# Performance work log

Measured on AMD Instinct MI355X. Metric: run time of the kernel, lower is better.

The kernel has to match this reference:

```python
import jax, jax.numpy as jnp
import numpy as np

B, H, S, D = 4, 16, 2048, 64


def setup_inputs() -> dict:
    key = jax.random.key(0)
    kq, kk, kv = jax.random.split(key, 3)
    q = jax.random.normal(kq, (B, H, S, D), dtype=jnp.float32)
    k = jax.random.normal(kk, (B, H, S, D), dtype=jnp.float32)
    v = jax.random.normal(kv, (B, H, S, D), dtype=jnp.float32)
    mask = jnp.tril(jnp.ones((S, S), dtype=jnp.bool_))  # causal: True = attend
    return {"q": q, "k": k, "v": v, "mask": mask}


def reference(q, k, v, mask):
    d_k = q.shape[-1]
    scale = 1.0 / jnp.sqrt(jnp.asarray(d_k, q.dtype))
    # scores: [B, H, S_q, S_k] -- full O(N^2) matrix, faithful to original
    score = jnp.einsum('bhqd,bhkd->bhqk', q, k) * scale
    score = jnp.where(mask, score, jnp.asarray(-jnp.inf, score.dtype))
    attn = jax.nn.softmax(score, axis=-1)
    return jnp.einsum('bhqk,bhkd->bhqd', attn, v)
```

## Files before the change

kernel.cpp:

```cpp
#include <hip/hip_runtime.h>
#include <hip/hip_bf16.h>

typedef __attribute__((ext_vector_type(8))) short short8_t;
typedef __attribute__((ext_vector_type(16))) float f32x16;
typedef __attribute__((ext_vector_type(4))) unsigned uint4_t;

constexpr int S  = 2048;
constexpr int D  = 64;
constexpr int BQ = 128;
constexpr int KV = 64;
constexpr int NQ = S / BQ;
constexpr int NT = S / KV;
constexpr float THR = 8.f;

static __device__ __forceinline__ unsigned packbf(float lo, float hi) {
  __hip_bfloat162 p = __float22bfloat162_rn(float2{lo, hi});
  return (unsigned)__bfloat16_as_ushort(p.x) | ((unsigned)__bfloat16_as_ushort(p.y) << 16);
}
static __device__ __forceinline__ short8_t pack8(float4 a, float4 b) {
  uint4_t u = { packbf(a.x, a.y), packbf(a.z, a.w), packbf(b.x, b.y), packbf(b.z, b.w) };
  return __builtin_bit_cast(short8_t, u);
}
static __device__ __forceinline__ float vmax16(const f32x16& a) {
  float x0 = fmaxf(a[0], a[1]),   x1 = fmaxf(a[2], a[3]);
  float x2 = fmaxf(a[4], a[5]),   x3 = fmaxf(a[6], a[7]);
  float x4 = fmaxf(a[8], a[9]),   x5 = fmaxf(a[10], a[11]);
  float x6 = fmaxf(a[12], a[13]), x7 = fmaxf(a[14], a[15]);
  x0 = fmaxf(x0, x1); x2 = fmaxf(x2, x3); x4 = fmaxf(x4, x5); x6 = fmaxf(x6, x7);
  return fmaxf(fmaxf(x0, x2), fmaxf(x4, x6));
}

static __device__ __forceinline__ void build_pfrags(const f32x16& p, int h,
                                                    short8_t& f0, short8_t& f1) {
  unsigned W0 = packbf(p[0],  p[1]),  W1 = packbf(p[2],  p[3]);
  unsigned W2 = packbf(p[4],  p[5]),  W3 = packbf(p[6],  p[7]);
  unsigned W4 = packbf(p[8],  p[9]),  W5 = packbf(p[10], p[11]);
  unsigned W6 = packbf(p[12], p[13]), W7 = packbf(p[14], p[15]);
  unsigned e0 = __shfl_xor(W0, 32), e1 = __shfl_xor(W1, 32);
  unsigned e2 = __shfl_xor(W2, 32), e3 = __shfl_xor(W3, 32);
  unsigned e4 = __shfl_xor(W4, 32), e5 = __shfl_xor(W5, 32);
  unsigned e6 = __shfl_xor(W6, 32), e7 = __shfl_xor(W7, 32);
  uint4_t u0, u1;
  if (h) { u0 = uint4_t{e2, e3, W2, W3}; u1 = uint4_t{e6, e7, W6, W7}; }
  else   { u0 = uint4_t{W0, W1, e0, e1}; u1 = uint4_t{W4, W5, e4, e5}; }
  f0 = __builtin_bit_cast(short8_t, u0);
  f1 = __builtin_bit_cast(short8_t, u1);
}

__global__ __launch_bounds__(256)
void prep_kernel(const float* __restrict__ k, const float* __restrict__ v,
                 short* __restrict__ kb, short* __restrict__ vtb)
{
  const int tile = (int)blockIdx.x;
  const int bh   = (int)blockIdx.y;
  const int tid  = (int)threadIdx.x;
  const int kv0  = tile * KV;
  const int srow = tid >> 2, sch = tid & 3;

  __shared__ float vt[KV][D + 4];

  {
    const float* kp = k + ((size_t)bh * S + kv0 + srow) * D + sch * 16;
    float4 a0 = *(const float4*)(kp);     float4 a1 = *(const float4*)(kp + 4);
    float4 a2 = *(const float4*)(kp + 8); float4 a3 = *(const float4*)(kp + 12);
    short* kd = kb + ((size_t)bh * S + kv0 + srow) * D;
    *(short8_t*)&kd[((2 * sch)     ^ (srow & 7)) * 8] = pack8(a0, a1);
    *(short8_t*)&kd[((2 * sch + 1) ^ (srow & 7)) * 8] = pack8(a2, a3);

    const float* vp = v + ((size_t)bh * S + kv0 + srow) * D + sch * 16;
    float4 b0 = *(const float4*)(vp);     float4 b1 = *(const float4*)(vp + 4);
    float4 b2 = *(const float4*)(vp + 8); float4 b3 = *(const float4*)(vp + 12);
    *(float4*)&vt[srow][sch * 16 + 0]  = b0;
    *(float4*)&vt[srow][sch * 16 + 4]  = b1;
    *(float4*)&vt[srow][sch * 16 + 8]  = b2;
    *(float4*)&vt[srow][sch * 16 + 12] = b3;
  }
  __syncthreads();
  {
    const int d = tid >> 2, q4 = tid & 3;
    float f[16];
    #pragma unroll
    for (int jj = 0; jj < 16; ++jj) f[jj] = vt[16 * q4 + jj][d];
    float4 c0 = make_float4(f[0],  f[1],  f[2],  f[3]);
    float4 c1 = make_float4(f[4],  f[5],  f[6],  f[7]);
    float4 c2 = make_float4(f[8],  f[9],  f[10], f[11]);
    float4 c3 = make_float4(f[12], f[13], f[14], f[15]);
    short* vd = vtb + (size_t)bh * S * D + (size_t)tile * KV * D + d * 64;
    *(short8_t*)&vd[((2 * q4)     ^ (d & 7)) * 8] = pack8(c0, c1);
    *(short8_t*)&vd[((2 * q4 + 1) ^ (d & 7)) * 8] = pack8(c2, c3);
  }
}

__global__ __launch_bounds__(256, 2)
void fattn4_kernel(const float* __restrict__ q, const short* __restrict__ kb,
                   const short* __restrict__ vtb, float* __restrict__ out)
{
  const int pair = (int)blockIdx.x;
  const int bh   = (int)blockIdx.y;
  const int tid  = (int)threadIdx.x;
  const int wave = tid >> 6;
  const int lane = tid & 63;
  const int h    = lane >> 5;
  const int ln   = lane & 31;

  __shared__ short bufK[2][KV * D];
  __shared__ short bufV[2][KV * D];

  const int nt0 = 2 * (pair + 1);
  const int ntt = nt0 + 2 * (NQ - pair);
  const short* kbase = kb  + (size_t)bh * S * D;
  const short* vbase = vtb + (size_t)bh * S * D;

  short8_t rk0, rk1, rv0, rv1;
  auto issue = [&](int t) {
    const short* gk = kbase + (size_t)t * (KV * D) + tid * 16;
    rk0 = *(const short8_t*)gk; rk1 = *(const short8_t*)(gk + 8);
    const short* gv = vbase + (size_t)t * (KV * D) + tid * 16;
    rv0 = *(const short8_t*)gv; rv1 = *(const short8_t*)(gv + 8);
  };
  issue(0);
  int cur = 0, j = 0;

  const float qscale = 0.125f * 1.4426950408889634f;

  #pragma unroll 1
  for (int seg = 0; seg < 2; ++seg) {
    const int qblk = seg ? (NQ - 1 - pair) : pair;
    const int qb = qblk * BQ;
    const int qw = qb + wave * 32;
    const int qi = qw + ln;
    const int qmax_w = qw + 31;
    const int ntseg = 2 * (qblk + 1);

    short8_t aq[4];
    {
      const float* qp = q + ((size_t)bh * S + qi) * D + 8 * h;
      #pragma unroll
      for (int ks = 0; ks < 4; ++ks) {
        float4 lo = *(const float4*)(qp + 16 * ks);
        float4 hi = *(const float4*)(qp + 16 * ks + 4);
        lo.x *= qscale; lo.y *= qscale; lo.z *= qscale; lo.w *= qscale;
        hi.x *= qscale; hi.y *= qscale; hi.z *= qscale; hi.w *= qscale;
        aq[ks] = pack8(lo, hi);
      }
    }

    f32x16 o0, o1;
    #pragma unroll
    for (int r = 0; r < 16; ++r) { o0[r] = 0.f; o1[r] = 0.f; }
    float m = -INFINITY, lsum = 0.f;

    #pragma unroll 1
    for (int i = 0; i < ntseg; ++i) {
      {
        short* dK = &bufK[cur][tid * 16];
        *(short8_t*)dK = rk0; *(short8_t*)(dK + 8) = rk1;
        short* dV = &bufV[cur][tid * 16];
        *(short8_t*)dV = rv0; *(short8_t*)(dV + 8) = rv1;
      }
      ++j;
      if (j < ntt) issue(j < nt0 ? j : j - nt0);
      __syncthreads();

      const int kv0 = i * KV;
      if (kv0 <= qmax_w) {
        const bool hi_live = (kv0 + 32 <= qmax_w);
        const short* Kc = bufK[cur];
        const short* Vc = bufV[cur];

        f32x16 st0, st1;
        #pragma unroll
        for (int r = 0; r < 16; ++r) { st0[r] = 0.f; st1[r] = 0.f; }
        #pragma unroll
        for (int ks = 0; ks < 4; ++ks) {
          short8_t kf0 = *(const short8_t*)&Kc[ln * D + (((2 * ks + h) ^ (ln & 7)) * 8)];
          st0 = __builtin_amdgcn_mfma_f32_32x32x16_bf16(kf0, aq[ks], st0, 0, 0, 0);
        }
        if (hi_live) {
          #pragma unroll
          for (int ks = 0; ks < 4; ++ks) {
            short8_t kf1 = *(const short8_t*)&Kc[(32 + ln) * D + (((2 * ks + h) ^ (ln & 7)) * 8)];
            st1 = __builtin_amdgcn_mfma_f32_32x32x16_bf16(kf1, aq[ks], st1, 0, 0, 0);
          }
        }

        if (kv0 + KV - 1 > qw) {
          #pragma unroll
          for (int r = 0; r < 16; ++r) {
            const int kvr = kv0 + (r & 3) + 8 * (r >> 2) + 4 * h;
            st0[r] = (kvr > qi) ? -INFINITY : st0[r];
            if (hi_live) st1[r] = (kvr + 32 > qi) ? -INFINITY : st1[r];
          }
        }

        float tm = hi_live ? fmaxf(vmax16(st0), vmax16(st1)) : vmax16(st0);
        tm = fmaxf(tm, __shfl_xor(tm, 32));
        if (!__all(tm <= m + THR)) {
          const float mn = fmaxf(m, tm);
          const float al = exp2f(m - mn);
          m = mn;
          lsum *= al;
          #pragma unroll
          for (int r = 0; r < 16; ++r) { o0[r] *= al; o1[r] *= al; }
        }
        float ssum = 0.f;
        #pragma unroll
        for (int r = 0; r < 16; ++r) { st0[r] = exp2f(st0[r] - m); ssum += st0[r]; }
        if (hi_live) {
          #pragma unroll
          for (int r = 0; r < 16; ++r) { st1[r] = exp2f(st1[r] - m); ssum += st1[r]; }
        }
        ssum += __shfl_xor(ssum, 32);
        lsum += ssum;

        short8_t p00, p01, p10, p11;
        build_pfrags(st0, h, p00, p01);
        if (hi_live) build_pfrags(st1, h, p10, p11);
        #pragma unroll
        for (int dt = 0; dt < 2; ++dt) {
          const int dr = 32 * dt + ln;
          f32x16 &o = dt ? o1 : o0;
          short8_t vf00 = *(const short8_t*)&Vc[dr * 64 + (((0 + h) ^ (dr & 7)) * 8)];
          short8_t vf01 = *(const short8_t*)&Vc[dr * 64 + (((2 + h) ^ (dr & 7)) * 8)];
          o = __builtin_amdgcn_mfma_f32_32x32x16_bf16(vf00, p00, o, 0, 0, 0);
          o = __builtin_amdgcn_mfma_f32_32x32x16_bf16(vf01, p01, o, 0, 0, 0);
          if (hi_live) {
            short8_t vf10 = *(const short8_t*)&Vc[dr * 64 + (((4 + h) ^ (dr & 7)) * 8)];
            short8_t vf11 = *(const short8_t*)&Vc[dr * 64 + (((6 + h) ^ (dr & 7)) * 8)];
            o = __builtin_amdgcn_mfma_f32_32x32x16_bf16(vf10, p10, o, 0, 0, 0);
            o = __builtin_amdgcn_mfma_f32_32x32x16_bf16(vf11, p11, o, 0, 0, 0);
          }
        }
      }
      cur ^= 1;
    }

    const float inv = 1.f / fmaxf(lsum, 1e-37f);
    float* op = out + ((size_t)bh * S + qi) * D;
    #pragma unroll
    for (int r = 0; r < 16; ++r) {
      const int dr = (r & 3) + 8 * (r >> 2) + 4 * h;
      op[dr]      = o0[r] * inv;
      op[32 + dr] = o1[r] * inv;
    }
  }
}

__global__ __launch_bounds__(256, 2)
void fattn3_kernel(const float* __restrict__ q, const float* __restrict__ k,
                   const float* __restrict__ v, float* __restrict__ out)
{
  const int pair = (int)blockIdx.x;
  const int bh   = (int)blockIdx.y;
  const int tid  = (int)threadIdx.x;
  const int wave = tid >> 6;
  const int lane = tid & 63;
  const int h    = lane >> 5;
  const int ln   = lane & 31;

  __shared__ short smem[BQ * D];
  short* Ks = smem;
  short* Vs = smem + KV * D;

  const float qscale = 0.125f * 1.4426950408889634f;
  const int srow = tid >> 2;
  const int sch  = tid & 3;

  #pragma unroll 1
  for (int seg = 0; seg < 2; ++seg) {
    const int qblk = seg ? (NQ - 1 - pair) : pair;
    const int qb = qblk * BQ;
    const int qw = qb + wave * 32;
    const int qi = qw + ln;
    const int qmax_w = qw + 31;
    const int kv_end = qb + BQ;

    __syncthreads();
    {
      const int r  = tid >> 1;
      const int h2 = tid & 1;
      const float* qp = q + ((size_t)bh * S + qb + r) * D + h2 * 32;
      #pragma unroll
      for (int jq = 0; jq < 4; ++jq) {
        float4 a = *(const float4*)(qp + jq * 8);
        float4 b = *(const float4*)(qp + jq * 8 + 4);
        a.x *= qscale; a.y *= qscale; a.z *= qscale; a.w *= qscale;
        b.x *= qscale; b.y *= qscale; b.z *= qscale; b.w *= qscale;
        *(short8_t*)&smem[r * D + (((4 * h2 + jq) ^ (r & 7)) * 8)] = pack8(a, b);
      }
    }
    __syncthreads();

    short8_t aq[4];
    {
      const int R = wave * 32 + ln;
      #pragma unroll
      for (int ks = 0; ks < 4; ++ks)
        aq[ks] = *(const short8_t*)&smem[R * D + (((2 * ks + h) ^ (R & 7)) * 8)];
    }
    __syncthreads();

    f32x16 o0, o1;
    #pragma unroll
    for (int r = 0; r < 16; ++r) { o0[r] = 0.f; o1[r] = 0.f; }
    float m = -INFINITY, lsum = 0.f;

    for (int kv0 = 0; kv0 < kv_end; kv0 += KV) {
      const float* kp = k + ((size_t)bh * S + kv0 + srow) * D + sch * 16;
      const float* vp = v + ((size_t)bh * S + kv0 + srow) * D + sch * 16;
      float4 k0 = *(const float4*)(kp);     float4 k1 = *(const float4*)(kp + 4);
      float4 k2 = *(const float4*)(kp + 8); float4 k3 = *(const float4*)(kp + 12);
      float4 v0 = *(const float4*)(vp);     float4 v1 = *(const float4*)(vp + 4);
      float4 v2 = *(const float4*)(vp + 8); float4 v3 = *(const float4*)(vp + 12);

      __syncthreads();
      *(short8_t*)&Ks[srow * D + (((2 * sch)     ^ (srow & 7)) * 8)] = pack8(k0, k1);
      *(short8_t*)&Ks[srow * D + (((2 * sch + 1) ^ (srow & 7)) * 8)] = pack8(k2, k3);
      {
        float vf[16] = { v0.x,v0.y,v0.z,v0.w, v1.x,v1.y,v1.z,v1.w,
                         v2.x,v2.y,v2.z,v2.w, v3.x,v3.y,v3.z,v3.w };
        #pragma unroll
        for (int jv = 0; jv < 16; jv += 2) {
          const unsigned pw = packbf(vf[jv], vf[jv + 1]);
          const int d0 = 16 * sch + jv, d1 = d0 + 1;
          Vs[d0 * 64 + (((srow >> 3) ^ (d0 & 7)) * 8) + (srow & 7)] = (short)(pw & 0xffffu);
          Vs[d1 * 64 + (((srow >> 3) ^ (d1 & 7)) * 8) + (srow & 7)] = (short)(pw >> 16);
        }
      }
      __syncthreads();

      if (kv0 <= qmax_w) {
        const bool hi_live = (kv0 + 32 <= qmax_w);
        f32x16 st0, st1;
        #pragma unroll
        for (int r = 0; r < 16; ++r) { st0[r] = 0.f; st1[r] = 0.f; }
        #pragma unroll
        for (int ks = 0; ks < 4; ++ks) {
          short8_t kf0 = *(const short8_t*)&Ks[ln * D + (((2 * ks + h) ^ (ln & 7)) * 8)];
          st0 = __builtin_amdgcn_mfma_f32_32x32x16_bf16(kf0, aq[ks], st0, 0, 0, 0);
        }
        if (hi_live) {
          #pragma unroll
          for (int ks = 0; ks < 4; ++ks) {
            short8_t kf1 = *(const short8_t*)&Ks[(32 + ln) * D + (((2 * ks + h) ^ (ln & 7)) * 8)];
            st1 = __builtin_amdgcn_mfma_f32_32x32x16_bf16(kf1, aq[ks], st1, 0, 0, 0);
          }
        }
        if (kv0 + KV - 1 > qw) {
          #pragma unroll
          for (int r = 0; r < 16; ++r) {
            const int kvr = kv0 + (r & 3) + 8 * (r >> 2) + 4 * h;
            st0[r] = (kvr > qi) ? -INFINITY : st0[r];
            if (hi_live) st1[r] = (kvr + 32 > qi) ? -INFINITY : st1[r];
          }
        }
        float tm = hi_live ? fmaxf(vmax16(st0), vmax16(st1)) : vmax16(st0);
        tm = fmaxf(tm, __shfl_xor(tm, 32));
        if (!__all(tm <= m + THR)) {
          const float mn = fmaxf(m, tm);
          const float al = exp2f(m - mn);
          m = mn;
          lsum *= al;
          #pragma unroll
          for (int r = 0; r < 16; ++r) { o0[r] *= al; o1[r] *= al; }
        }
        float ssum = 0.f;
        #pragma unroll
        for (int r = 0; r < 16; ++r) { st0[r] = exp2f(st0[r] - m); ssum += st0[r]; }
        if (hi_live) {
          #pragma unroll
          for (int r = 0; r < 16; ++r) { st1[r] = exp2f(st1[r] - m); ssum += st1[r]; }
        }
        ssum += __shfl_xor(ssum, 32);
        lsum += ssum;

        short8_t p00, p01, p10, p11;
        build_pfrags(st0, h, p00, p01);
        if (hi_live) build_pfrags(st1, h, p10, p11);
        #pragma unroll
        for (int dt = 0; dt < 2; ++dt) {
          const int dr = 32 * dt + ln;
          f32x16 &o = dt ? o1 : o0;
          short8_t vf00 = *(const short8_t*)&Vs[dr * 64 + (((0 + h) ^ (dr & 7)) * 8)];
          short8_t vf01 = *(const short8_t*)&Vs[dr * 64 + (((2 + h) ^ (dr & 7)) * 8)];
          o = __builtin_amdgcn_mfma_f32_32x32x16_bf16(vf00, p00, o, 0, 0, 0);
          o = __builtin_amdgcn_mfma_f32_32x32x16_bf16(vf01, p01, o, 0, 0, 0);
          if (hi_live) {
            short8_t vf10 = *(const short8_t*)&Vs[dr * 64 + (((4 + h) ^ (dr & 7)) * 8)];
            short8_t vf11 = *(const short8_t*)&Vs[dr * 64 + (((6 + h) ^ (dr & 7)) * 8)];
            o = __builtin_amdgcn_mfma_f32_32x32x16_bf16(vf10, p10, o, 0, 0, 0);
            o = __builtin_amdgcn_mfma_f32_32x32x16_bf16(vf11, p11, o, 0, 0, 0);
          }
        }
      }
    }

    const float inv = 1.f / fmaxf(lsum, 1e-37f);
    float* op = out + ((size_t)bh * S + qi) * D;
    #pragma unroll
    for (int r = 0; r < 16; ++r) {
      const int dr = (r & 3) + 8 * (r >> 2) + 4 * h;
      op[dr]      = o0[r] * inv;
      op[32 + dr] = o1[r] * inv;
    }
  }
}

extern "C" void kernel_launch(void* const* d_in, const int* in_sizes, int n_in,
                              void* d_out, int out_size, void* d_ws, size_t ws_size,
                              hipStream_t stream) {
  const float* q = (const float*)d_in[0];
  const float* k = (const float*)d_in[1];
  const float* v = (const float*)d_in[2];
  float* out = (float*)d_out;
  const int BH = in_sizes[0] / (S * D);
  const size_t need = (size_t)BH * S * D * 2  * 2 ;
  if (ws_size >= need) {
    short* kbw  = (short*)d_ws;
    short* vtbw = kbw + (size_t)BH * S * D;
    prep_kernel<<<dim3(NT, BH), 256, 0, stream>>>(k, v, kbw, vtbw);
    fattn4_kernel<<<dim3(NQ / 2, BH), 256, 0, stream>>>(q, kbw, vtbw, out);
  } else {
    fattn3_kernel<<<dim3(NQ / 2, BH), 256, 0, stream>>>(q, k, v, out);
  }
}
```

Baseline: 103.4 us.

## Double query rows per wave to reuse K/V tiles across two Q subtiles

The main attention kernel now assigns 64 query rows per wave (two 32-row subtiles A and B), so each query block grows to 256 rows. Each K fragment loaded from LDS and each V fragment is reused for two MFMA chains, which halves shared-memory reads per FLOP and halves the number of times K/V tiles are streamed per head. The causal mask is simplified to a diagonal-tile check. In exchange it doubles accumulator registers (risking occupancy or spills under the 2-block launch bound), halves the grid to 4 blocks per head (256 blocks total), and makes causal load balancing coarser.

```diff
diff --git a/kernel.cpp b/kernel.cpp
--- a/kernel.cpp
+++ b/kernel.cpp
@@ -7,11 +7,13 @@
 
 constexpr int S  = 2048;
 constexpr int D  = 64;
-constexpr int BQ = 128;
 constexpr int KV = 64;
-constexpr int NQ = S / BQ;
 constexpr int NT = S / KV;
+constexpr int BH_C = 64;
 constexpr float THR = 8.f;
+
+constexpr int BQ7 = 256;
+constexpr int NQ7 = S / BQ7;
 
 static __device__ __forceinline__ unsigned packbf(float lo, float hi) {
   __hip_bfloat162 p = __float22bfloat162_rn(float2{lo, hi});
@@ -47,6 +49,30 @@
   f1 = __builtin_bit_cast(short8_t, u1);
 }
 
+static __device__ __forceinline__ void online_sm(f32x16& st0, f32x16& st1, bool hi,
+                                                 float& m, float& lsum,
+                                                 f32x16& o0, f32x16& o1) {
+  float tm = hi ? fmaxf(vmax16(st0), vmax16(st1)) : vmax16(st0);
+  tm = fmaxf(tm, __shfl_xor(tm, 32));
+  if (!__all(tm <= m + THR)) {
+    const float mn = fmaxf(m, tm);
+    const float al = exp2f(m - mn);
+    m = mn;
+    lsum *= al;
+    #pragma unroll
+    for (int r = 0; r < 16; ++r) { o0[r] *= al; o1[r] *= al; }
+  }
+  float ssum = 0.f;
+  #pragma unroll
+  for (int r = 0; r < 16; ++r) { st0[r] = exp2f(st0[r] - m); ssum += st0[r]; }
+  if (hi) {
+    #pragma unroll
+    for (int r = 0; r < 16; ++r) { st1[r] = exp2f(st1[r] - m); ssum += st1[r]; }
+  }
+  ssum += __shfl_xor(ssum, 32);
+  lsum += ssum;
+}
+
 __global__ __launch_bounds__(256)
 void prep_kernel(const float* __restrict__ k, const float* __restrict__ v,
                  short* __restrict__ kb, short* __restrict__ vtb)
@@ -92,7 +118,7 @@
 }
 
 __global__ __launch_bounds__(256, 2)
-void fattn4_kernel(const float* __restrict__ q, const short* __restrict__ kb,
+void fattn7_kernel(const float* __restrict__ q, const short* __restrict__ kb,
                    const short* __restrict__ vtb, float* __restrict__ out)
 {
   const int pair = (int)blockIdx.x;
@@ -106,8 +132,8 @@
   __shared__ short bufK[2][KV * D];
   __shared__ short bufV[2][KV * D];
 
-  const int nt0 = 2 * (pair + 1);
-  const int ntt = nt0 + 2 * (NQ - pair);
+  const int nt0 = 4 * (pair + 1);
+  const int ntt = nt0 + 4 * (8 - pair);
   const short* kbase = kb  + (size_t)bh * S * D;
   const short* vbase = vtb + (size_t)bh * S * D;
 
@@ -125,30 +151,40 @@
 
   #pragma unroll 1
   for (int seg = 0; seg < 2; ++seg) {
-    const int qblk = seg ? (NQ - 1 - pair) : pair;
-    const int qb = qblk * BQ;
-    const int qw = qb + wave * 32;
-    const int qi = qw + ln;
-    const int qmax_w = qw + 31;
-    const int ntseg = 2 * (qblk + 1);
-
-    short8_t aq[4];
+    const int qblk = seg ? (7 - pair) : pair;
+    const int qb = qblk * BQ7;
+    const int qw = qb + wave * 64;
+    const int qA = qw + ln;
+    const int qB = qw + 32 + ln;
+    const int ntseg = 4 * (qblk + 1);
+    const int nlive = (qw >> 6) + 1;
+
+    short8_t aqA[4], aqB[4];
     {
-      const float* qp = q + ((size_t)bh * S + qi) * D + 8 * h;
+      const float* qpA = q + ((size_t)bh * S + qA) * D + 8 * h;
+      const float* qpB = q + ((size_t)bh * S + qB) * D + 8 * h;
       #pragma unroll
       for (int ks = 0; ks < 4; ++ks) {
-        float4 lo = *(const float4*)(qp + 16 * ks);
-        float4 hi = *(const float4*)(qp + 16 * ks + 4);
+        float4 lo = *(const float4*)(qpA + 16 * ks);
+        float4 hi = *(const float4*)(qpA + 16 * ks + 4);
         lo.x *= qscale; lo.y *= qscale; lo.z *= qscale; lo.w *= qscale;
         hi.x *= qscale; hi.y *= qscale; hi.z *= qscale; hi.w *= qscale;
-        aq[ks] = pack8(lo, hi);
-      }
-    }
-
-    f32x16 o0, o1;
-    #pragma unroll
-    for (int r = 0; r < 16; ++r) { o0[r] = 0.f; o1[r] = 0.f; }
-    float m = -INFINITY, lsum = 0.f;
+        aqA[ks] = pack8(lo, hi);
+      }
+      #pragma unroll
+      for (int ks = 0; ks < 4; ++ks) {
+        float4 lo = *(const float4*)(qpB + 16 * ks);
+        float4 hi = *(const float4*)(qpB + 16 * ks + 4);
+        lo.x *= qscale; lo.y *= qscale; lo.z *= qscale; lo.w *= qscale;
+        hi.x *= qscale; hi.y *= qscale; hi.z *= qscale; hi.w *= qscale;
+        aqB[ks] = pack8(lo, hi);
+      }
+    }
+
+    f32x16 oA0, oA1, oB0, oB1;
+    #pragma unroll
+    for (int r = 0; r < 16; ++r) { oA0[r] = 0.f; oA1[r] = 0.f; oB0[r] = 0.f; oB1[r] = 0.f; }
+    float mA = -INFINITY, lA = 0.f, mB = -INFINITY, lB = 0.f;
 
     #pragma unroll 1
     for (int i = 0; i < ntseg; ++i) {
@@ -162,86 +198,108 @@
       if (j < ntt) issue(j < nt0 ? j : j - nt0);
       __syncthreads();
 
-      const int kv0 = i * KV;
-      if (kv0 <= qmax_w) {
-        const bool hi_live = (kv0 + 32 <= qmax_w);
+      if (i < nlive) {
+        const bool diag = (i == nlive - 1);
         const short* Kc = bufK[cur];
         const short* Vc = bufV[cur];
 
-        f32x16 st0, st1;
-        #pragma unroll
-        for (int r = 0; r < 16; ++r) { st0[r] = 0.f; st1[r] = 0.f; }
-        #pragma unroll
-        for (int ks = 0; ks < 4; ++ks) {
-          short8_t kf0 = *(const short8_t*)&Kc[ln * D + (((2 * ks + h) ^ (ln & 7)) * 8)];
-          st0 = __builtin_amdgcn_mfma_f32_32x32x16_bf16(kf0, aq[ks], st0, 0, 0, 0);
-        }
-        if (hi_live) {
-          #pragma unroll
-          for (int ks = 0; ks < 4; ++ks) {
-            short8_t kf1 = *(const short8_t*)&Kc[(32 + ln) * D + (((2 * ks + h) ^ (ln & 7)) * 8)];
-            st1 = __builtin_amdgcn_mfma_f32_32x32x16_bf16(kf1, aq[ks], st1, 0, 0, 0);
-          }
-        }
-
-        if (kv0 + KV - 1 > qw) {
-          #pragma unroll
-          for (int r = 0; r < 16; ++r) {
-            const int kvr = kv0 + (r & 3) + 8 * (r >> 2) + 4 * h;
-            st0[r] = (kvr > qi) ? -INFINITY : st0[r];
-            if (hi_live) st1[r] = (kvr + 32 > qi) ? -INFINITY : st1[r];
-          }
-        }
-
-        float tm = hi_live ? fmaxf(vmax16(st0), vmax16(st1)) : vmax16(st0);
-        tm = fmaxf(tm, __shfl_xor(tm, 32));
-        if (!__all(tm <= m + THR)) {
-          const float mn = fmaxf(m, tm);
-          const float al = exp2f(m - mn);
-          m = mn;
-          lsum *= al;
-          #pragma unroll
-          for (int r = 0; r < 16; ++r) { o0[r] *= al; o1[r] *= al; }
-        }
-        float ssum = 0.f;
-        #pragma unroll
-        for (int r = 0; r < 16; ++r) { st0[r] = exp2f(st0[r] - m); ssum += st0[r]; }
-        if (hi_live) {
-          #pragma unroll
-          for (int r = 0; r < 16; ++r) { st1[r] = exp2f(st1[r] - m); ssum += st1[r]; }
-        }
-        ssum += __shfl_xor(ssum, 32);
-        lsum += ssum;
-
-        short8_t p00, p01, p10, p11;
-        build_pfrags(st0, h, p00, p01);
-        if (hi_live) build_pfrags(st1, h, p10, p11);
+        short8_t kf0[4], kf1[4];
+        #pragma unroll
+        for (int ks = 0; ks < 4; ++ks)
+          kf0[ks] = *(const short8_t*)&Kc[ln * D + (((2 * ks + h) ^ (ln & 7)) * 8)];
+        #pragma unroll
+        for (int ks = 0; ks < 4; ++ks)
+          kf1[ks] = *(const short8_t*)&Kc[(32 + ln) * D + (((2 * ks + h) ^ (ln & 7)) * 8)];
+
+
+        short8_t pA0, pA1, pA2, pA3;
+        {
+          f32x16 stA0, stA1;
+          #pragma unroll
+          for (int r = 0; r < 16; ++r) { stA0[r] = 0.f; stA1[r] = 0.f; }
+          #pragma unroll
+          for (int ks = 0; ks < 4; ++ks)
+            stA0 = __builtin_amdgcn_mfma_f32_32x32x16_bf16(kf0[ks], aqA[ks], stA0, 0, 0, 0);
+          if (!diag) {
+            #pragma unroll
+            for (int ks = 0; ks < 4; ++ks)
+              stA1 = __builtin_amdgcn_mfma_f32_32x32x16_bf16(kf1[ks], aqA[ks], stA1, 0, 0, 0);
+          } else {
+            #pragma unroll
+            for (int r = 0; r < 16; ++r) {
+              const int crow = (r & 3) + 8 * (r >> 2) + 4 * h;
+              stA0[r] = (crow > ln) ? -INFINITY : stA0[r];
+            }
+          }
+          online_sm(stA0, stA1, !diag, mA, lA, oA0, oA1);
+          build_pfrags(stA0, h, pA0, pA1);
+          if (!diag) build_pfrags(stA1, h, pA2, pA3);
+        }
+
+        short8_t pB0, pB1, pB2, pB3;
+        {
+          f32x16 stB0, stB1;
+          #pragma unroll
+          for (int r = 0; r < 16; ++r) { stB0[r] = 0.f; stB1[r] = 0.f; }
+          #pragma unroll
+          for (int ks = 0; ks < 4; ++ks)
+            stB0 = __builtin_amdgcn_mfma_f32_32x32x16_bf16(kf0[ks], aqB[ks], stB0, 0, 0, 0);
+          #pragma unroll
+          for (int ks = 0; ks < 4; ++ks)
+            stB1 = __builtin_amdgcn_mfma_f32_32x32x16_bf16(kf1[ks], aqB[ks], stB1, 0, 0, 0);
+          if (diag) {
+            #pragma unroll
+            for (int r = 0; r < 16; ++r) {
+              const int crow = (r & 3) + 8 * (r >> 2) + 4 * h;
+              stB1[r] = (crow > ln) ? -INFINITY : stB1[r];
+            }
+          }
+          online_sm(stB0, stB1, true, mB, lB, oB0, oB1);
+          build_pfrags(stB0, h, pB0, pB1);
+          build_pfrags(stB1, h, pB2, pB3);
+        }
+
         #pragma unroll
         for (int dt = 0; dt < 2; ++dt) {
           const int dr = 32 * dt + ln;
-          f32x16 &o = dt ? o1 : o0;
-          short8_t vf00 = *(const short8_t*)&Vc[dr * 64 + (((0 + h) ^ (dr & 7)) * 8)];
-          short8_t vf01 = *(const short8_t*)&Vc[dr * 64 + (((2 + h) ^ (dr & 7)) * 8)];
-          o = __builtin_amdgcn_mfma_f32_32x32x16_bf16(vf00, p00, o, 0, 0, 0);
-          o = __builtin_amdgcn_mfma_f32_32x32x16_bf16(vf01, p01, o, 0, 0, 0);
-          if (hi_live) {
-            short8_t vf10 = *(const short8_t*)&Vc[dr * 64 + (((4 + h) ^ (dr & 7)) * 8)];
-            short8_t vf11 = *(const short8_t*)&Vc[dr * 64 + (((6 + h) ^ (dr & 7)) * 8)];
-            o = __builtin_amdgcn_mfma_f32_32x32x16_bf16(vf10, p10, o, 0, 0, 0);
-            o = __builtin_amdgcn_mfma_f32_32x32x16_bf16(vf11, p11, o, 0, 0, 0);
-          }
+          f32x16 &oa = dt ? oA1 : oA0;
+          f32x16 &ob = dt ? oB1 : oB0;
+          short8_t vf0 = *(const short8_t*)&Vc[dr * 64 + (((0 + h) ^ (dr & 7)) * 8)];
+          short8_t vf1 = *(const short8_t*)&Vc[dr * 64 + (((2 + h) ^ (dr & 7)) * 8)];
+          oa = __builtin_amdgcn_mfma_f32_32x32x16_bf16(vf0, pA0, oa, 0, 0, 0);
+          oa = __builtin_amdgcn_mfma_f32_32x32x16_bf16(vf1, pA1, oa, 0, 0, 0);
+          ob = __builtin_amdgcn_mfma_f32_32x32x16_bf16(vf0, pB0, ob, 0, 0, 0);
+          ob = __builtin_amdgcn_mfma_f32_32x32x16_bf16(vf1, pB1, ob, 0, 0, 0);
+          short8_t vf2 = *(const short8_t*)&Vc[dr * 64 + (((4 + h) ^ (dr & 7)) * 8)];
+          short8_t vf3 = *(const short8_t*)&Vc[dr * 64 + (((6 + h) ^ (dr & 7)) * 8)];
+          if (!diag) {
+            oa = __builtin_amdgcn_mfma_f32_32x32x16_bf16(vf2, pA2, oa, 0, 0, 0);
+            oa = __builtin_amdgcn_mfma_f32_32x32x16_bf16(vf3, pA3, oa, 0, 0, 0);
+          }
+          ob = __builtin_amdgcn_mfma_f32_32x32x16_bf16(vf2, pB2, ob, 0, 0, 0);
+          ob = __builtin_amdgcn_mfma_f32_32x32x16_bf16(vf3, pB3, ob, 0, 0, 0);
         }
       }
       cur ^= 1;
     }
 
-    const float inv = 1.f / fmaxf(lsum, 1e-37f);
-    float* op = out + ((size_t)bh * S + qi) * D;
-    #pragma unroll
-    for (int r = 0; r < 16; ++r) {
-      const int dr = (r & 3) + 8 * (r >> 2) + 4 * h;
-      op[dr]      = o0[r] * inv;
-      op[32 + dr] = o1[r] * inv;
+    {
+      const float invA = 1.f / fmaxf(lA, 1e-37f);
+      float* opA = out + ((size_t)bh * S + qA) * D;
+      #pragma unroll
+      for (int r = 0; r < 16; ++r) {
+        const int dr = (r & 3) + 8 * (r >> 2) + 4 * h;
+        opA[dr]      = oA0[r] * invA;
+        opA[32 + dr] = oA1[r] * invA;
+      }
+      const float invB = 1.f / fmaxf(lB, 1e-37f);
+      float* opB = out + ((size_t)bh * S + qB) * D;
+      #pragma unroll
+      for (int r = 0; r < 16; ++r) {
+        const int dr = (r & 3) + 8 * (r >> 2) + 4 * h;
+        opB[dr]      = oB0[r] * invB;
+        opB[32 + dr] = oB1[r] * invB;
+      }
     }
   }
 }
@@ -250,6 +308,8 @@
 void fattn3_kernel(const float* __restrict__ q, const float* __restrict__ k,
                    const float* __restrict__ v, float* __restrict__ out)
 {
+  constexpr int BQ = 128;
+  constexpr int NQ = S / BQ;
   const int pair = (int)blockIdx.x;
   const int bh   = (int)blockIdx.y;
   const int tid  = (int)threadIdx.x;
@@ -354,25 +414,7 @@
             if (hi_live) st1[r] = (kvr + 32 > qi) ? -INFINITY : st1[r];
           }
         }
-        float tm = hi_live ? fmaxf(vmax16(st0), vmax16(st1)) : vmax16(st0);
-        tm = fmaxf(tm, __shfl_xor(tm, 32));
-        if (!__all(tm <= m + THR)) {
-          const float mn = fmaxf(m, tm);
-          const float al = exp2f(m - mn);
-          m = mn;
-          lsum *= al;
-          #pragma unroll
-          for (int r = 0; r < 16; ++r) { o0[r] *= al; o1[r] *= al; }
-        }
-        float ssum = 0.f;
-        #pragma unroll
-        for (int r = 0; r < 16; ++r) { st0[r] = exp2f(st0[r] - m); ssum += st0[r]; }
-        if (hi_live) {
-          #pragma unroll
-          for (int r = 0; r < 16; ++r) { st1[r] = exp2f(st1[r] - m); ssum += st1[r]; }
-        }
-        ssum += __shfl_xor(ssum, 32);
-        lsum += ssum;
+        online_sm(st0, st1, hi_live, m, lsum, o0, o1);
 
         short8_t p00, p01, p10, p11;
         build_pfrags(st0, h, p00, p01);
@@ -415,12 +457,12 @@
   float* out = (float*)d_out;
   const int BH = in_sizes[0] / (S * D);
   const size_t need = (size_t)BH * S * D * 2  * 2 ;
-  if (ws_size >= need) {
+  if (ws_size >= need && BH == BH_C) {
     short* kbw  = (short*)d_ws;
     short* vtbw = kbw + (size_t)BH * S * D;
     prep_kernel<<<dim3(NT, BH), 256, 0, stream>>>(k, v, kbw, vtbw);
-    fattn4_kernel<<<dim3(NQ / 2, BH), 256, 0, stream>>>(q, kbw, vtbw, out);
+    fattn7_kernel<<<dim3(NQ7 / 2, BH), 256, 0, stream>>>(q, kbw, vtbw, out);
   } else {
-    fattn3_kernel<<<dim3(NQ / 2, BH), 256, 0, stream>>>(q, k, v, out);
-  }
-}
+    fattn3_kernel<<<dim3((S / 128) / 2, BH), 256, 0, stream>>>(q, k, v, out);
+  }
+}
```

After: 123.6 us. 19.4% more time.
